# Optimization experiments

Measured on AMD Instinct MI355X. Metric: run time of the kernel, lower is better.

## Reference

```python
import jax, jax.numpy as jnp
import numpy as np

B, T, C, HS = 64, 256, 2048, 128


def setup_inputs() -> dict:
    key = jax.random.key(0)
    k1, k2, k3, k4 = jax.random.split(key, 4)
    x = jax.random.normal(k1, (B, T, C), dtype=jnp.float32)
    # Dense(head_size, use_bias=False) kernels, scaled like glorot-ish init
    Wk = jax.random.normal(k2, (C, HS), dtype=jnp.float32) * (C ** -0.5)
    Wq = jax.random.normal(k3, (C, HS), dtype=jnp.float32) * (C ** -0.5)
    Wv = jax.random.normal(k4, (C, HS), dtype=jnp.float32) * (C ** -0.5)
    return {"x": x, "Wk": Wk, "Wq": Wq, "Wv": Wv}


def reference(x, Wk, Wq, Wv):
    Bn, Tn, Cn = x.shape
    k = jnp.einsum("btc,ch->bth", x, Wk)
    q = jnp.einsum("btc,ch->bth", x, Wq)
    v = jnp.einsum("btc,ch->bth", x, Wv)
    # faithful to source: scores = k @ q^T, scaled by C**-0.5 (input dim!)
    scores = jnp.einsum("bth,bsh->bts", k, q) * (Cn ** -0.5)
    causal = jnp.tril(jnp.ones((Tn, Tn), dtype=bool))  # [T, T]
    scores = jnp.where(causal, scores, -jnp.inf)
    weights = jax.nn.softmax(scores, axis=-1)
    return jnp.einsum("bts,bsh->bth", weights, v)
```

## Files before the change

kernel.cpp:

```cpp
#include <hip/hip_runtime.h>
#include <hip/hip_bf16.h>
#include <cstdint>
#include <cstddef>

#define B_  64
#define T_  256
#define C_  2048
#define HS_ 128
#define N_  384

typedef __bf16 bf16x8 __attribute__((ext_vector_type(8)));
typedef float  floatx4 __attribute__((ext_vector_type(4)));

__device__ __forceinline__ unsigned short f2bf_rne(float f) {
  union { float f; unsigned int u; } v; v.f = f;
  unsigned int r = v.u + 0x7fffu + ((v.u >> 16) & 1u);
  return (unsigned short)(r >> 16);
}
__device__ __forceinline__ unsigned short f2bf(float f) {
  union { float f; unsigned int u; } v; v.f = f;
  return (unsigned short)((v.u + 0x8000u) >> 16);
}

__device__ __forceinline__ void async_copy16(const void* g, void* l) {
  __builtin_amdgcn_global_load_lds(
      (const __attribute__((address_space(1))) unsigned int*)g,
      (__attribute__((address_space(3))) unsigned int*)l, 16, 0, 0);
}

__global__ __launch_bounds__(256) void wt_kernel(
    const float* __restrict__ Wk, const float* __restrict__ Wq,
    const float* __restrict__ Wv, unsigned short* __restrict__ Wt) {
  __shared__ float tile[32][33];
  const int w  = blockIdx.z;
  const int c0 = blockIdx.x * 32;
  const int h0 = blockIdx.y * 32;
  const float* W = (w == 0) ? Wk : (w == 1) ? Wq : Wv;
  const int tx = threadIdx.x & 31, ty = threadIdx.x >> 5;
#pragma unroll
  for (int i = 0; i < 32; i += 8)
    tile[ty + i][tx] = W[(size_t)(c0 + ty + i) * HS_ + h0 + tx];
  __syncthreads();
#pragma unroll
  for (int i = 0; i < 32; i += 8) {
    int hh = ty + i, cc = tx;
    Wt[(size_t)(w * HS_ + h0 + hh) * C_ + c0 + cc] = f2bf_rne(tile[cc][hh]);
  }
}

__global__ __launch_bounds__(256, 4) void qkv_gemm(
    const float* __restrict__ X, const unsigned short* __restrict__ Wt,
    unsigned short* __restrict__ kqv, unsigned short* __restrict__ vT) {
  __shared__ unsigned short As[2][64 * 64];
  __shared__ unsigned short Bs[2][96 * 64];

  const int tid  = threadIdx.x;
  const int wave = tid >> 6, lane = tid & 63;
  const int quad = lane >> 4, l16 = lane & 15;

  const int g  = blockIdx.x;
  const int ml = g & 7;
  const int nb = (g >> 3) & 3;
  const int mh = g >> 5;
  const int m0 = (mh * 8 + ml) * 64;
  const int n0 = nb * 96;
  const int wm = (wave >> 1) * 32;
  const int wn = (wave & 1) * 48;

  const unsigned short* bsrc[3]; int bdst[3];
#pragma unroll
  for (int r = 0; r < 3; ++r) {
    int s = r * 256 + tid;
    int n = s >> 3, sl = s & 7;
    bsrc[r] = Wt + (size_t)(n0 + n) * C_ + (sl ^ (n & 7)) * 8;
    bdst[r] = (r * 256 + wave * 64) * 8;
  }
  int arow[4], achk[4], awoff[4];
#pragma unroll
  for (int r = 0; r < 4; ++r) {
    int s = r * 256 + tid;
    arow[r] = s >> 4; achk[r] = s & 15;
    awoff[r] = arow[r] * 64 + (((achk[r] >> 1) ^ (arow[r] & 7)) << 3) + ((achk[r] & 1) << 2);
  }

#pragma unroll
  for (int r = 0; r < 3; ++r)
    async_copy16(bsrc[r], &Bs[0][bdst[r]]);
  float4 av[4];
#pragma unroll
  for (int r = 0; r < 4; ++r)
    av[r] = *(const float4*)(X + (size_t)(m0 + arow[r]) * C_ + achk[r] * 4);

  floatx4 acc[2][3] = {};

  for (int k = 0; k < 32; ++k) {
    const int cur = k & 1, nxt = cur ^ 1;
#pragma unroll
    for (int r = 0; r < 4; ++r) {
      ushort4 b4;
      b4.x = f2bf(av[r].x); b4.y = f2bf(av[r].y);
      b4.z = f2bf(av[r].z); b4.w = f2bf(av[r].w);
      *(ushort4*)&As[cur][awoff[r]] = b4;
    }
    __syncthreads();

    if (k < 31) {
      const int kn = (k + 1) * 64;
#pragma unroll
      for (int r = 0; r < 3; ++r)
        async_copy16(bsrc[r] + kn, &Bs[nxt][bdst[r]]);
#pragma unroll
      for (int r = 0; r < 4; ++r)
        av[r] = *(const float4*)(X + (size_t)(m0 + arow[r]) * C_ + kn + achk[r] * 4);
    }

#pragma unroll
    for (int ks = 0; ks < 2; ++ks) {
      bf16x8 af[2], bfv[3];
#pragma unroll
      for (int mt = 0; mt < 2; ++mt) {
        int rr = wm + mt * 16 + l16;
        af[mt] = *(const bf16x8*)&As[cur][rr * 64 + (((ks * 4 + quad) ^ (rr & 7)) << 3)];
      }
#pragma unroll
      for (int nt = 0; nt < 3; ++nt) {
        int n = wn + nt * 16 + l16;
        bfv[nt] = *(const bf16x8*)&Bs[cur][n * 64 + (((ks * 4 + quad) ^ (n & 7)) << 3)];
      }
#pragma unroll
      for (int mt = 0; mt < 2; ++mt)
#pragma unroll
        for (int nt = 0; nt < 3; ++nt)
          acc[mt][nt] = __builtin_amdgcn_mfma_f32_16x16x32_bf16(
              af[mt], bfv[nt], acc[mt][nt], 0, 0, 0);
    }
  }

#pragma unroll
  for (int mt = 0; mt < 2; ++mt)
#pragma unroll
    for (int nt = 0; nt < 3; ++nt)
#pragma unroll
      for (int r = 0; r < 4; ++r) {
        int row = m0 + wm + mt * 16 + quad * 4 + r;
        int col = n0 + wn + nt * 16 + l16;
        unsigned short us = f2bf(acc[mt][nt][r]);
        kqv[(size_t)row * N_ + col] = us;
        if (col >= 256) {
          int bb = row >> 8, tt = row & 255;
          vT[(size_t)bb * HS_ * T_ + (size_t)(col - 256) * T_ + tt] = us;
        }
      }
}

__global__ __launch_bounds__(256) void attn_kernel(
    const unsigned short* __restrict__ kqv, const unsigned short* __restrict__ vT,
    float* __restrict__ out) {
  __shared__ unsigned short P[4][16 * 136];
  __shared__ float Olds[2][16][132];
  __shared__ float rs1[2][16];

  const int tid  = threadIdx.x;
  const int wave = tid >> 6, lane = tid & 63;
  const int quad = lane >> 4, l16 = lane & 15;
  const int tile = wave >> 1, par = wave & 1;
  const int tt = tile ? (15 - (int)blockIdx.x) : (int)blockIdx.x;
  const int b  = blockIdx.y;
  const int t0 = tt * 16;
  const float scale = 0.022097086912079612f;
  const unsigned short* kq = kqv + (size_t)b * T_ * N_;

  bf16x8 kf[4];
#pragma unroll
  for (int ks = 0; ks < 4; ++ks)
    kf[ks] = *(const bf16x8*)&kq[(size_t)(t0 + l16) * N_ + ks * 32 + quad * 8];

  const int n_my = ((tt + 1) + (1 - par)) >> 1;
  const int npad = (n_my + 1) & ~1;

  float rsum[4] = {0.f, 0.f, 0.f, 0.f};

  bf16x8 qf[4];
  if (n_my > 0) {
    const int st = par;
#pragma unroll
    for (int ks = 0; ks < 4; ++ks)
      qf[ks] = *(const bf16x8*)&kq[(size_t)(st * 16 + l16) * N_ + HS_ + ks * 32 + quad * 8];
  }
  for (int j = 0; j < n_my; ++j) {
    bf16x8 qn[4];
    if (j + 1 < n_my) {
      const int st = par + 2 * (j + 1);
#pragma unroll
      for (int ks = 0; ks < 4; ++ks)
        qn[ks] = *(const bf16x8*)&kq[(size_t)(st * 16 + l16) * N_ + HS_ + ks * 32 + quad * 8];
    }
    floatx4 a = {};
#pragma unroll
    for (int ks = 0; ks < 4; ++ks)
      a = __builtin_amdgcn_mfma_f32_16x16x32_bf16(kf[ks], qf[ks], a, 0, 0, 0);
    const int st = par + 2 * j;
    const int scol = st * 16 + l16;
#pragma unroll
    for (int r = 0; r < 4; ++r) {
      int trow = t0 + quad * 4 + r;
      float p = (scol <= trow) ? __expf(a[r] * scale) : 0.f;
      rsum[r] += p;
      P[wave][(quad * 4 + r) * 136 + j * 16 + l16] = f2bf(p);
    }
#pragma unroll
    for (int ks = 0; ks < 4; ++ks) qf[ks] = qn[ks];
  }
  if (npad > n_my) {
#pragma unroll
    for (int r = 0; r < 4; ++r)
      P[wave][(quad * 4 + r) * 136 + n_my * 16 + l16] = 0;
  }
#pragma unroll
  for (int m = 1; m < 16; m <<= 1)
#pragma unroll
    for (int r = 0; r < 4; ++r)
      rsum[r] += __shfl_xor(rsum[r], m, 64);

  floatx4 oacc[8] = {};
  const unsigned short* vb = vT + (size_t)b * HS_ * T_;
  const int nks = npad >> 1;
  const int sb_off = (quad >> 1);
  const int sb_lo  = (quad & 1) * 8;
  bf16x8 bv[8]; bf16x8 pa;
  if (nks > 0) {
    int st = par + 2 * (0 + sb_off);
    int sbase = st * 16 + sb_lo;
    pa = *(const bf16x8*)&P[wave][l16 * 136 + 0 * 32 + quad * 8];
#pragma unroll
    for (int nt = 0; nt < 8; ++nt)
      bv[nt] = *(const bf16x8*)&vb[(size_t)(nt * 16 + l16) * T_ + sbase];
  }
  for (int ks2 = 0; ks2 < nks; ++ks2) {
    bf16x8 bvn[8]; bf16x8 pan;
    if (ks2 + 1 < nks) {
      int jt = 2 * (ks2 + 1) + sb_off;
      int st = par + 2 * jt;
      int sbase = st * 16 + sb_lo;
      pan = *(const bf16x8*)&P[wave][l16 * 136 + (ks2 + 1) * 32 + quad * 8];
#pragma unroll
      for (int nt = 0; nt < 8; ++nt)
        bvn[nt] = *(const bf16x8*)&vb[(size_t)(nt * 16 + l16) * T_ + sbase];
    }
#pragma unroll
    for (int nt = 0; nt < 8; ++nt)
      oacc[nt] = __builtin_amdgcn_mfma_f32_16x16x32_bf16(pa, bv[nt], oacc[nt], 0, 0, 0);
    pa = pan;
#pragma unroll
    for (int nt = 0; nt < 8; ++nt) bv[nt] = bvn[nt];
  }

  if (par == 1) {
#pragma unroll
    for (int nt = 0; nt < 8; ++nt)
#pragma unroll
      for (int r = 0; r < 4; ++r)
        Olds[tile][quad * 4 + r][nt * 16 + l16] = oacc[nt][r];
    if (l16 == 0) {
#pragma unroll
      for (int r = 0; r < 4; ++r) rs1[tile][quad * 4 + r] = rsum[r];
    }
  }
  __syncthreads();
  if (par == 0) {
    float inv[4];
#pragma unroll
    for (int r = 0; r < 4; ++r)
      inv[r] = 1.f / (rsum[r] + rs1[tile][quad * 4 + r]);
    float* ob = out + ((size_t)b * T_ + t0) * HS_;
#pragma unroll
    for (int nt = 0; nt < 8; ++nt)
#pragma unroll
      for (int r = 0; r < 4; ++r) {
        int row = quad * 4 + r;
        ob[(size_t)row * HS_ + nt * 16 + l16] =
            (oacc[nt][r] + Olds[tile][row][nt * 16 + l16]) * inv[r];
      }
  }
}

extern "C" void kernel_launch(void* const* d_in, const int* in_sizes, int n_in,
                              void* d_out, int out_size, void* d_ws, size_t ws_size,
                              hipStream_t stream) {
  const float* x  = (const float*)d_in[0];
  const float* Wk = (const float*)d_in[1];
  const float* Wq = (const float*)d_in[2];
  const float* Wv = (const float*)d_in[3];
  float* out = (float*)d_out;

  char* ws = (char*)d_ws;
  unsigned short* Wt  = (unsigned short*)(ws);
  unsigned short* kqv = (unsigned short*)(ws + 1572864);
  unsigned short* vT  = (unsigned short*)(ws + 1572864 + 12582912);

  hipLaunchKernelGGL(wt_kernel, dim3(64, 4, 3), dim3(256), 0, stream, Wk, Wq, Wv, Wt);
  hipLaunchKernelGGL(qkv_gemm, dim3(1024), dim3(256), 0, stream, x, Wt, kqv, vT);
  hipLaunchKernelGGL(attn_kernel, dim3(8, 64), dim3(256), 0, stream, kqv, vT, out);
}
```

Baseline: 247.9 us.

## Widen QKV GEMM tile to cover all 384 output columns per block

The QKV projection GEMM now has each 512-thread block compute a 64x384 tile covering the full K/Q/V width, where before four blocks each computed 64x96. This means each row of X is loaded from global memory and converted to bf16 once instead of four times. The cost is 112 KB of dynamic LDS per block and a grid of only 256 blocks, which lowers occupancy to about one block per CU and limits latency hiding.

After: 232.0 us. 6.4% less time.

```diff
diff --git a/kernel.cpp b/kernel.cpp
--- a/kernel.cpp
+++ b/kernel.cpp
@@ -48,89 +48,85 @@
   }
 }
 
-__global__ __launch_bounds__(256, 4) void qkv_gemm(
+__global__ __launch_bounds__(512) void qkv_gemm(
     const float* __restrict__ X, const unsigned short* __restrict__ Wt,
     unsigned short* __restrict__ kqv, unsigned short* __restrict__ vT) {
-  __shared__ unsigned short As[2][64 * 64];
-  __shared__ unsigned short Bs[2][96 * 64];
+  extern __shared__ char smem[];
 
   const int tid  = threadIdx.x;
   const int wave = tid >> 6, lane = tid & 63;
   const int quad = lane >> 4, l16 = lane & 15;
 
-  const int g  = blockIdx.x;
-  const int ml = g & 7;
-  const int nb = (g >> 3) & 3;
-  const int mh = g >> 5;
-  const int m0 = (mh * 8 + ml) * 64;
-  const int n0 = nb * 96;
-  const int wm = (wave >> 1) * 32;
-  const int wn = (wave & 1) * 48;
-
-  const unsigned short* bsrc[3]; int bdst[3];
-#pragma unroll
-  for (int r = 0; r < 3; ++r) {
-    int s = r * 256 + tid;
+  const int m0 = blockIdx.x * 64;
+  const int wm = (wave >> 2) * 32;
+  const int wn = (wave & 3) * 96;
+
+  const unsigned short* bsrc[6]; int bdst[6];
+#pragma unroll
+  for (int r = 0; r < 6; ++r) {
+    int s = r * 512 + tid;
     int n = s >> 3, sl = s & 7;
-    bsrc[r] = Wt + (size_t)(n0 + n) * C_ + (sl ^ (n & 7)) * 8;
-    bdst[r] = (r * 256 + wave * 64) * 8;
-  }
-  int arow[4], achk[4], awoff[4];
-#pragma unroll
-  for (int r = 0; r < 4; ++r) {
-    int s = r * 256 + tid;
+    bsrc[r] = Wt + (size_t)n * C_ + (sl ^ (n & 7)) * 8;
+    bdst[r] = (r * 512 + wave * 64) * 16;
+  }
+  int arow[2], achk[2], awoff[2];
+#pragma unroll
+  for (int r = 0; r < 2; ++r) {
+    int s = r * 512 + tid;
     arow[r] = s >> 4; achk[r] = s & 15;
     awoff[r] = arow[r] * 64 + (((achk[r] >> 1) ^ (arow[r] & 7)) << 3) + ((achk[r] & 1) << 2);
   }
 
 #pragma unroll
-  for (int r = 0; r < 3; ++r)
-    async_copy16(bsrc[r], &Bs[0][bdst[r]]);
-  float4 av[4];
-#pragma unroll
-  for (int r = 0; r < 4; ++r)
+  for (int r = 0; r < 6; ++r)
+    async_copy16(bsrc[r], smem + bdst[r]);
+  float4 av[2];
+#pragma unroll
+  for (int r = 0; r < 2; ++r)
     av[r] = *(const float4*)(X + (size_t)(m0 + arow[r]) * C_ + achk[r] * 4);
 
-  floatx4 acc[2][3] = {};
+  floatx4 acc[2][6] = {};
 
   for (int k = 0; k < 32; ++k) {
     const int cur = k & 1, nxt = cur ^ 1;
-#pragma unroll
-    for (int r = 0; r < 4; ++r) {
+    unsigned short* As = (unsigned short*)(smem + 98304 + cur * 8192);
+#pragma unroll
+    for (int r = 0; r < 2; ++r) {
       ushort4 b4;
       b4.x = f2bf(av[r].x); b4.y = f2bf(av[r].y);
       b4.z = f2bf(av[r].z); b4.w = f2bf(av[r].w);
-      *(ushort4*)&As[cur][awoff[r]] = b4;
+      *(ushort4*)&As[awoff[r]] = b4;
     }
     __syncthreads();
 
     if (k < 31) {
       const int kn = (k + 1) * 64;
 #pragma unroll
-      for (int r = 0; r < 3; ++r)
-        async_copy16(bsrc[r] + kn, &Bs[nxt][bdst[r]]);
-#pragma unroll
-      for (int r = 0; r < 4; ++r)
+      for (int r = 0; r < 6; ++r)
+        async_copy16(bsrc[r] + kn, smem + nxt * 49152 + bdst[r]);
+#pragma unroll
+      for (int r = 0; r < 2; ++r)
         av[r] = *(const float4*)(X + (size_t)(m0 + arow[r]) * C_ + kn + achk[r] * 4);
     }
 
+    const unsigned short* Bsr = (const unsigned short*)(smem + cur * 49152);
 #pragma unroll
     for (int ks = 0; ks < 2; ++ks) {
-      bf16x8 af[2], bfv[3];
+      bf16x8 af[2], bfv[6];
 #pragma unroll
       for (int mt = 0; mt < 2; ++mt) {
         int rr = wm + mt * 16 + l16;
-        af[mt] = *(const bf16x8*)&As[cur][rr * 64 + (((ks * 4 + quad) ^ (rr & 7)) << 3)];
+        af[mt] = *(const bf16x8*)&As[rr * 64 + (((ks * 4 + quad) ^ (rr & 7)) << 3)];
       }
 #pragma unroll
-      for (int nt = 0; nt < 3; ++nt) {
+      for (int nt = 0; nt < 6; ++nt) {
         int n = wn + nt * 16 + l16;
-        bfv[nt] = *(const bf16x8*)&Bs[cur][n * 64 + (((ks * 4 + quad) ^ (n & 7)) << 3)];
+        bfv[nt] = *(const bf16x8*)&Bsr[n * 64 + (((ks * 4 + quad) ^ (n & 7)) << 3)];
       }
 #pragma unroll
       for (int mt = 0; mt < 2; ++mt)
 #pragma unroll
-        for (int nt = 0; nt < 3; ++nt)
+        for (int nt = 0; nt < 6; ++nt)
           acc[mt][nt] = __builtin_amdgcn_mfma_f32_16x16x32_bf16(
               af[mt], bfv[nt], acc[mt][nt], 0, 0, 0);
     }
@@ -139,11 +135,11 @@
 #pragma unroll
   for (int mt = 0; mt < 2; ++mt)
 #pragma unroll
-    for (int nt = 0; nt < 3; ++nt)
+    for (int nt = 0; nt < 6; ++nt)
 #pragma unroll
       for (int r = 0; r < 4; ++r) {
         int row = m0 + wm + mt * 16 + quad * 4 + r;
-        int col = n0 + wn + nt * 16 + l16;
+        int col = wn + nt * 16 + l16;
         unsigned short us = f2bf(acc[mt][nt][r]);
         kqv[(size_t)row * N_ + col] = us;
         if (col >= 256) {
@@ -298,7 +294,15 @@
   unsigned short* kqv = (unsigned short*)(ws + 1572864);
   unsigned short* vT  = (unsigned short*)(ws + 1572864 + 12582912);
 
+  static bool attr_set = false;
+  if (!attr_set) {
+    (void)hipFuncSetAttribute(reinterpret_cast<const void*>(qkv_gemm),
+                              hipFuncAttributeMaxDynamicSharedMemorySize,
+                              114688);
+    attr_set = true;
+  }
+
   hipLaunchKernelGGL(wt_kernel, dim3(64, 4, 3), dim3(256), 0, stream, Wk, Wq, Wv, Wt);
-  hipLaunchKernelGGL(qkv_gemm, dim3(1024), dim3(256), 0, stream, x, Wt, kqv, vT);
+  hipLaunchKernelGGL(qkv_gemm, dim3(256), dim3(512), 114688, stream, x, Wt, kqv, vT);
   hipLaunchKernelGGL(attn_kernel, dim3(8, 64), dim3(256), 0, stream, kqv, vT, out);
 }
```
